# Performance work log

Measured on AMD Instinct MI355X. Metric: run time of the kernel, lower is better.

The kernel has to match this reference:

```python
import jax, jax.numpy as jnp
import numpy as np

SR = 16000
N_FFT = 400
HOP = 160
N_MELS = 128
F_MIN = 0.0
F_MAX = 8000.0
PCEN_ALPHA = 0.8
PCEN_SMOOTH = 0.04
PCEN_DELTA = 2.0
PCEN_ROOT = 2.0
PCEN_FLOOR = 1e-08
TARGET = (192, 128)


def _hz_to_mel(f):
    return 2595.0 * np.log10(1.0 + f / 700.0)


def _mel_to_hz(m):
    return 700.0 * (10.0 ** (m / 2595.0) - 1.0)


def _mel_filterbank():
    # torchaudio melscale_fbanks, mel_scale='htk', norm=None
    n_freqs = N_FFT // 2 + 1  # 201
    all_freqs = np.linspace(0.0, SR / 2, n_freqs)
    m_pts = np.linspace(_hz_to_mel(F_MIN), _hz_to_mel(F_MAX), N_MELS + 2)
    f_pts = _mel_to_hz(m_pts)
    f_diff = f_pts[1:] - f_pts[:-1]  # (n_mels+1,)
    slopes = f_pts[None, :] - all_freqs[:, None]  # (n_freqs, n_mels+2)
    down = -slopes[:, :-2] / f_diff[:-1]
    up = slopes[:, 2:] / f_diff[1:]
    fb = np.maximum(0.0, np.minimum(down, up))  # (n_freqs, n_mels)
    return jnp.asarray(fb, dtype=jnp.float32)


def _hann_window():
    # periodic hann, matches torch.hann_window(400)
    n = np.arange(N_FFT)
    return jnp.asarray(0.5 * (1.0 - np.cos(2.0 * np.pi * n / N_FFT)), dtype=jnp.float32)


def setup_inputs() -> dict:
    key = jax.random.key(0)
    audio = jax.random.normal(key, (2048, 32000), dtype=jnp.float32)
    return {"audio": audio}


def _mel_spectrogram(audio):
    # center=True reflect pad by n_fft//2
    pad = N_FFT // 2
    x = jnp.pad(audio, ((0, 0), (pad, pad)), mode='reflect')  # (N, 32400)
    T = (x.shape[1] - N_FFT) // HOP + 1  # 201
    idx = jnp.arange(T)[:, None] * HOP + jnp.arange(N_FFT)[None, :]  # (T, n_fft)
    frames = x[:, idx] * _hann_window()  # (N, T, n_fft)
    spec = jnp.fft.rfft(frames, axis=-1)  # (N, T, 201)
    power = jnp.abs(spec) ** 2
    mel = jnp.einsum('ntf,fm->ntm', power, _mel_filterbank())  # (N, T, n_mels)
    return mel


def _pcen(mel_ntm):
    # IIR smoothing over time via scan; mel_ntm: (N, T, M)
    s = PCEN_SMOOTH
    mel_t = jnp.transpose(mel_ntm, (1, 0, 2))  # (T, N, M)

    def step(m_prev, e):
        m_new = (1.0 - s) * m_prev + s * e
        return m_new, m_new

    m0 = mel_t[0]
    _, Ms = jax.lax.scan(step, m0, mel_t[1:])
    M = jnp.concatenate([m0[None], Ms], axis=0)  # (T, N, Mels)
    M = jnp.transpose(M, (1, 0, 2))  # (N, T, Mels)
    inv_r = 1.0 / PCEN_ROOT
    return (mel_ntm / (PCEN_FLOOR + M) ** PCEN_ALPHA + PCEN_DELTA) ** inv_r - PCEN_DELTA ** inv_r


def reference(audio):
    mel = _mel_spectrogram(audio)          # (N, T, 128); original is (N,128,T), PCEN over time either way
    pcen = _pcen(mel)                      # (N, T, 128) == original after transpose(1,2)
    x = pcen[:, None, :, :]                # (N, 1, T, 128)
    N = x.shape[0]
    # bilinear, align_corners=False == jax.image 'linear' (half-pixel centers)
    out = jax.image.resize(x, (N, 1, TARGET[0], TARGET[1]), method='linear')
    return out
```

## Files before the change

kernel.cpp:

```cpp
#include <hip/hip_runtime.h>
#include <math.h>

typedef __attribute__((ext_vector_type(8))) _Float16 half8;
typedef __attribute__((ext_vector_type(4))) float f32x4;
typedef __attribute__((ext_vector_type(4))) unsigned int u32x4;

namespace {
constexpr int NS = 32000, PAD = 200, NT = 201, TOUT = 192, NMEL = 128;
constexpr int PW_STRIDE = 236;
constexpr int BAS_NT = 28;
constexpr int BAS_ELEMS = 13 * 28 * 64 * 8;
constexpr int FB_ELEMS  = 7 * 8 * 64 * 8;
constexpr int OUT_ROW_U16 = TOUT * NMEL * 2;
constexpr int MEL_OFF_U16 = OUT_ROW_U16 - NT * NMEL;
}

__device__ __forceinline__ int swz(int e) { return e ^ (((e >> 7) & 3) << 3); }
__device__ __forceinline__ unsigned short f2h(float f) {
  _Float16 h = (_Float16)f; return __builtin_bit_cast(unsigned short, h);
}
__device__ __forceinline__ float h2f(unsigned short u) {
  return (float)__builtin_bit_cast(_Float16, u);
}

__global__ void setup_tables(unsigned short* __restrict__ ws) {
  int idx = blockIdx.x * 256 + threadIdx.x;
  if (idx < BAS_ELEMS) {
    int j = idx & 7, lane = (idx >> 3) & 63, rest = idx >> 9;
    int nt = rest % BAS_NT, ks = rest / BAS_NT;
    int k   = ks * 32 + ((lane >> 4) << 3) + j;
    int col = nt * 16 + (lane & 15);
    float v = 0.f;
    if (k < 400 && col < 402) {
      int bin = col >> 1;
      int mm  = (k * bin) % 400;
      float th = (float)mm * 0.015707963267948967f;
      float tr = (col & 1) ? sinf(th) : cosf(th);
      float wn = 0.5f * (1.0f - cosf((float)k * 0.015707963267948967f));
      v = wn * tr;
    }
    ws[idx] = f2h(v);
  } else if (idx < BAS_ELEMS + FB_ELEMS) {
    int i2 = idx - BAS_ELEMS;
    int j = i2 & 7, lane = (i2 >> 3) & 63, rest = i2 >> 9;
    int nt = rest % 8, ks = rest / 8;
    int k   = ks * 32 + ((lane >> 4) << 3) + j;
    int mel = nt * 16 + (lane & 15);
    float v = 0.f;
    if (k <= 200) {
      double mhi = 2595.0 * log10(1.0 + 8000.0 / 700.0);
      double ml = mhi * (double)mel / 129.0;
      double mc = mhi * (double)(mel + 1) / 129.0;
      double mr = mhi * (double)(mel + 2) / 129.0;
      double fl = 700.0 * (pow(10.0, ml / 2595.0) - 1.0);
      double fc = 700.0 * (pow(10.0, mc / 2595.0) - 1.0);
      double fr = 700.0 * (pow(10.0, mr / 2595.0) - 1.0);
      double f  = 40.0 * (double)k;
      double wv = fmin((f - fl) / (fc - fl), (fr - f) / (fr - fc));
      v = (float)fmax(0.0, wv);
    }
    ws[idx] = f2h(v);
  }
}

template <int MT>
__global__ __launch_bounds__(256) __attribute__((amdgpu_waves_per_eu(3)))
void dft_mel_kernel(const float* __restrict__ audio, const unsigned short* __restrict__ ws,
                    unsigned short* __restrict__ outu)
{
  constexpr int AU = (MT == 3) ? 7936 : 2816;
  __shared__ unsigned short au[AU];
  __shared__ unsigned short pw16[MT * 16 * PW_STRIDE];
  const int tid = threadIdx.x;
  const int bid = blockIdx.x;
  const int r  = (MT == 3) ? (bid >> 2) : bid;
  const int t0 = (MT == 3) ? ((bid & 3) * 48) : 192;
  const float* __restrict__ ab = audio + (size_t)r * NS;
  const int g0 = t0 * 160 - PAD;

  {
    constexpr int nchunk = AU / 8;
    #pragma unroll 4
    for (int ci = tid; ci < nchunk; ci += 256) {
      half8 hv;
      int gbase = g0 + ci * 8;
      if (gbase >= 0 && gbase + 7 < NS) {
        const float4* p = (const float4*)(ab + gbase);
        float4 x0 = p[0], x1 = p[1];
        hv[0] = (_Float16)x0.x; hv[1] = (_Float16)x0.y;
        hv[2] = (_Float16)x0.z; hv[3] = (_Float16)x0.w;
        hv[4] = (_Float16)x1.x; hv[5] = (_Float16)x1.y;
        hv[6] = (_Float16)x1.z; hv[7] = (_Float16)x1.w;
      } else {
        #pragma unroll
        for (int j = 0; j < 8; ++j) {
          int g = gbase + j;
          if (g < 0) g = -g;
          if (g >= NS) g = 2 * NS - 2 - g;
          hv[j] = (_Float16)ab[g];
        }
      }
      *(half8*)(au + swz(ci * 8)) = hv;
    }
  }
  __syncthreads();

  const int w = tid >> 6, lane = tid & 63, lr = lane & 15, lg = lane >> 4;

  f32x4 acc[MT][7];
  #pragma unroll
  for (int mm = 0; mm < MT; ++mm)
    #pragma unroll
    for (int n = 0; n < 7; ++n) acc[mm][n] = (f32x4){0.f, 0.f, 0.f, 0.f};
  {
    const int laneA = lr * 160 + lg * 8;
    const unsigned short* bptr = ws + ((size_t)(w * 7 * 64 + lane)) * 8;
    half8 Bcur = *(const half8*)bptr;
    for (int ks = 0; ks < 13; ++ks) {
      half8 Af[MT];
      #pragma unroll
      for (int mm = 0; mm < MT; ++mm)
        Af[mm] = *(const half8*)(au + swz(mm * 2560 + ks * 32 + laneA));
      #pragma unroll
      for (int n = 0; n < 7; ++n) {
        half8 Bnext = Bcur;
        if (n < 6)        Bnext = *(const half8*)(bptr + (n + 1) * 512);
        else if (ks < 12) Bnext = *(const half8*)(bptr + BAS_NT * 512);
        #pragma unroll
        for (int mm = 0; mm < MT; ++mm)
          acc[mm][n] = __builtin_amdgcn_mfma_f32_16x16x32_f16(Af[mm], Bcur, acc[mm][n], 0, 0, 0);
        Bcur = Bnext;
      }
      bptr += BAS_NT * 512;
    }
  }
  __syncthreads();

  #pragma unroll
  for (int mm = 0; mm < MT; ++mm) {
    #pragma unroll
    for (int n = 0; n < 7; ++n) {
      int gcol = (w * 7 + n) * 16 + lr;
      int bin  = gcol >> 1;
      float p[4];
      #pragma unroll
      for (int j = 0; j < 4; ++j) {
        float v = acc[mm][n][j];
        int iv = __builtin_bit_cast(int, v);
        float q = __builtin_bit_cast(float,
            __builtin_amdgcn_mov_dpp(iv, 0xB1, 0xF, 0xF, true));
        p[j] = fmaf(v, v, q * q);
      }
      bool odd = (lr & 1);
      int rowb = mm * 16 + lg * 4 + (odd ? 2 : 0);
      pw16[rowb * PW_STRIDE + bin]       = f2h(odd ? p[2] : p[0]);
      pw16[(rowb + 1) * PW_STRIDE + bin] = f2h(odd ? p[3] : p[1]);
    }
  }
  __syncthreads();

  {
    half8 Fb[2][7];
    const unsigned short* fbase = ws + BAS_ELEMS + (size_t)lane * 8;
    #pragma unroll
    for (int nt = 0; nt < 2; ++nt)
      #pragma unroll
      for (int ks = 0; ks < 7; ++ks)
        Fb[nt][ks] = *(const half8*)(fbase + ((size_t)(ks * 8 + 2 * w + nt)) * 512);
    #pragma unroll
    for (int mt = 0; mt < MT; ++mt) {
      half8 Pa[7];
      const unsigned short* psrc = pw16 + (mt * 16 + lr) * PW_STRIDE + lg * 8;
      #pragma unroll
      for (int ks = 0; ks < 7; ++ks) Pa[ks] = *(const half8*)(psrc + ks * 32);
      #pragma unroll
      for (int nt = 0; nt < 2; ++nt) {
        f32x4 a2 = (f32x4){0.f, 0.f, 0.f, 0.f};
        #pragma unroll
        for (int ks = 0; ks < 7; ++ks)
          a2 = __builtin_amdgcn_mfma_f32_16x16x32_f16(Pa[ks], Fb[nt][ks], a2, 0, 0, 0);
        int gm = (2 * w + nt) * 16 + lr;
        #pragma unroll
        for (int j = 0; j < 4; ++j) {
          int t = t0 + mt * 16 + lg * 4 + j;
          if (MT == 3 || t < NT)
            outu[(size_t)r * OUT_ROW_U16 + MEL_OFF_U16 + t * NMEL + gm] = f2h(a2[j]);
        }
      }
    }
  }
}

__global__ __launch_bounds__(512)
void pcen_resize_kernel(unsigned short* __restrict__ outu)
{
  __shared__ unsigned short mel[NT * NMEL];
  __shared__ float carry[4][NMEL];
  __shared__ float minb[4][NMEL];
  const int tid = threadIdx.x;
  const int r = blockIdx.x;
  const unsigned short* src = outu + (size_t)r * OUT_ROW_U16 + MEL_OFF_U16;
  for (int i = tid; i < (NT * NMEL) / 8; i += 512)
    *(u32x4*)(mel + i * 8) = *(const u32x4*)(src + (size_t)i * 8);
  __syncthreads();

  const int m = tid & 127, c = tid >> 7;
  const int t0  = (c == 0) ? 0 : (51 + 50 * (c - 1));
  const int len = (c == 0) ? 51 : 50;

  float M = 0.f;
  for (int t = t0; t < t0 + len; ++t) {
    float e = h2f(mel[t * NMEL + m]);
    M = (t == 0) ? e : fmaf(0.96f, M, 0.04f * e);
  }
  carry[c][m] = M;
  __syncthreads();
  if (c == 0) {
    float a50 = exp2f(50.0f * log2f(0.96f));
    float m1 = carry[0][m];
    float m2 = fmaf(a50, m1, carry[1][m]);
    float m3 = fmaf(a50, m2, carry[2][m]);
    minb[1][m] = m1; minb[2][m] = m2; minb[3][m] = m3;
  }
  __syncthreads();

  float Min = (c == 0) ? 0.f : minb[c][m];
  float wf = 1.f, Mloc = 0.f;
  for (int t = t0; t < t0 + len; ++t) {
    float e = h2f(mel[t * NMEL + m]);
    Mloc = (t == 0) ? e : fmaf(0.96f, Mloc, 0.04f * e);
    wf *= 0.96f;
    float Mt = fmaf(wf, Min, Mloc);
    float dn = exp2f(0.8f * log2f(1e-8f + Mt));
    float pc = sqrtf(e / dn + 2.0f) - 1.41421356237309515f;
    mel[t * NMEL + m] = f2h(pc);
  }
  __syncthreads();

  float* __restrict__ ob = (float*)outu + (size_t)r * TOUT * NMEL;
  const float INVS = 201.0f / 192.0f;
  for (int i = c; i < TOUT; i += 4) {
    float ct = ((float)i + 0.5f) * INVS - 0.5f;
    int jlo = (int)ceilf(ct - INVS);
    int jhi = (int)floorf(ct + INVS);
    if (jlo < 0) jlo = 0;
    if (jhi > NT - 1) jhi = NT - 1;
    float wsum = 0.f, val = 0.f;
    for (int j = jlo; j <= jhi; ++j) {
      float wv = 1.0f - fabsf((float)j - ct) / INVS;
      if (wv > 0.f) { wsum += wv; val = fmaf(wv, h2f(mel[j * NMEL + m]), val); }
    }
    ob[(size_t)i * NMEL + m] = val / wsum;
  }
}

extern "C" void kernel_launch(void* const* d_in, const int* in_sizes, int n_in,
                              void* d_out, int out_size, void* d_ws, size_t ws_size,
                              hipStream_t stream) {
  (void)in_sizes; (void)n_in; (void)out_size; (void)ws_size;
  unsigned short* ws = (unsigned short*)d_ws;
  setup_tables<<<(BAS_ELEMS + FB_ELEMS + 255) / 256, 256, 0, stream>>>(ws);
  dft_mel_kernel<3><<<2048 * 4, 256, 0, stream>>>((const float*)d_in[0], ws,
                                                  (unsigned short*)d_out);
  dft_mel_kernel<1><<<2048, 256, 0, stream>>>((const float*)d_in[0], ws,
                                              (unsigned short*)d_out);
  pcen_resize_kernel<<<2048, 512, 0, stream>>>((unsigned short*)d_out);
}
```

Before: 464.7 us.

## Merge DFT-mel launches into one kernel with aliased LDS; widen PCEN scan

The two templated DFT/mel launches (one for the 48-frame tiles, one for the tail frames) become a single launch of 5 blocks per row, dispatching on block index. The audio staging buffer and the power buffer now share one LDS allocation, which cuts shared memory per block. The amdgpu_waves_per_eu(3) attribute is dropped, which may change register allocation. The PCEN/resize kernel moves from 512 to 1024 threads, splitting the time scan into 8 chunks with a longer carry-propagation chain, to expose more parallelism per row.

Result: faster. 454.3 us (-2.2%).

```diff
diff --git a/kernel.cpp b/kernel.cpp
--- a/kernel.cpp
+++ b/kernel.cpp
@@ -13,6 +13,7 @@
 constexpr int FB_ELEMS  = 7 * 8 * 64 * 8;
 constexpr int OUT_ROW_U16 = TOUT * NMEL * 2;
 constexpr int MEL_OFF_U16 = OUT_ROW_U16 - NT * NMEL;
+constexpr int BUF_U16 = 48 * PW_STRIDE;
 }
 
 __device__ __forceinline__ int swz(int e) { return e ^ (((e >> 7) & 3) << 3); }
@@ -64,18 +65,11 @@
 }
 
 template <int MT>
-__global__ __launch_bounds__(256) __attribute__((amdgpu_waves_per_eu(3)))
-void dft_mel_kernel(const float* __restrict__ audio, const unsigned short* __restrict__ ws,
-                    unsigned short* __restrict__ outu)
+__device__ __forceinline__ void dft_mel_body(const float* __restrict__ ab,
+    const unsigned short* __restrict__ ws, unsigned short* __restrict__ outrow,
+    unsigned short* __restrict__ buf, int t0, int tid)
 {
   constexpr int AU = (MT == 3) ? 7936 : 2816;
-  __shared__ unsigned short au[AU];
-  __shared__ unsigned short pw16[MT * 16 * PW_STRIDE];
-  const int tid = threadIdx.x;
-  const int bid = blockIdx.x;
-  const int r  = (MT == 3) ? (bid >> 2) : bid;
-  const int t0 = (MT == 3) ? ((bid & 3) * 48) : 192;
-  const float* __restrict__ ab = audio + (size_t)r * NS;
   const int g0 = t0 * 160 - PAD;
 
   {
@@ -100,7 +94,7 @@
           hv[j] = (_Float16)ab[g];
         }
       }
-      *(half8*)(au + swz(ci * 8)) = hv;
+      *(half8*)(buf + swz(ci * 8)) = hv;
     }
   }
   __syncthreads();
@@ -120,7 +114,7 @@
       half8 Af[MT];
       #pragma unroll
       for (int mm = 0; mm < MT; ++mm)
-        Af[mm] = *(const half8*)(au + swz(mm * 2560 + ks * 32 + laneA));
+        Af[mm] = *(const half8*)(buf + swz(mm * 2560 + ks * 32 + laneA));
       #pragma unroll
       for (int n = 0; n < 7; ++n) {
         half8 Bnext = Bcur;
@@ -136,6 +130,7 @@
   }
   __syncthreads();
 
+  unsigned short* pw16 = buf;
   #pragma unroll
   for (int mm = 0; mm < MT; ++mm) {
     #pragma unroll
@@ -184,29 +179,42 @@
         for (int j = 0; j < 4; ++j) {
           int t = t0 + mt * 16 + lg * 4 + j;
           if (MT == 3 || t < NT)
-            outu[(size_t)r * OUT_ROW_U16 + MEL_OFF_U16 + t * NMEL + gm] = f2h(a2[j]);
+            outrow[t * NMEL + gm] = f2h(a2[j]);
         }
       }
     }
   }
 }
 
-__global__ __launch_bounds__(512)
+__global__ __launch_bounds__(256)
+void dft_mel_kernel(const float* __restrict__ audio, const unsigned short* __restrict__ ws,
+                    unsigned short* __restrict__ outu)
+{
+  __shared__ unsigned short buf[BUF_U16];
+  const int bid = blockIdx.x;
+  const int r = bid / 5, s = bid - r * 5;
+  const float* __restrict__ ab = audio + (size_t)r * NS;
+  unsigned short* outrow = outu + (size_t)r * OUT_ROW_U16 + MEL_OFF_U16;
+  if (s < 4) dft_mel_body<3>(ab, ws, outrow, buf, s * 48, threadIdx.x);
+  else       dft_mel_body<1>(ab, ws, outrow, buf, 192, threadIdx.x);
+}
+
+__global__ __launch_bounds__(1024)
 void pcen_resize_kernel(unsigned short* __restrict__ outu)
 {
   __shared__ unsigned short mel[NT * NMEL];
-  __shared__ float carry[4][NMEL];
-  __shared__ float minb[4][NMEL];
+  __shared__ float carry[8][NMEL];
+  __shared__ float minb[8][NMEL];
   const int tid = threadIdx.x;
   const int r = blockIdx.x;
   const unsigned short* src = outu + (size_t)r * OUT_ROW_U16 + MEL_OFF_U16;
-  for (int i = tid; i < (NT * NMEL) / 8; i += 512)
+  for (int i = tid; i < (NT * NMEL) / 8; i += 1024)
     *(u32x4*)(mel + i * 8) = *(const u32x4*)(src + (size_t)i * 8);
   __syncthreads();
 
   const int m = tid & 127, c = tid >> 7;
-  const int t0  = (c == 0) ? 0 : (51 + 50 * (c - 1));
-  const int len = (c == 0) ? 51 : 50;
+  const int t0  = (c == 0) ? 0 : (26 + 25 * (c - 1));
+  const int len = (c == 0) ? 26 : 25;
 
   float M = 0.f;
   for (int t = t0; t < t0 + len; ++t) {
@@ -216,11 +224,14 @@
   carry[c][m] = M;
   __syncthreads();
   if (c == 0) {
-    float a50 = exp2f(50.0f * log2f(0.96f));
-    float m1 = carry[0][m];
-    float m2 = fmaf(a50, m1, carry[1][m]);
-    float m3 = fmaf(a50, m2, carry[2][m]);
-    minb[1][m] = m1; minb[2][m] = m2; minb[3][m] = m3;
+    float a25 = exp2f(25.0f * log2f(0.96f));
+    float acc = carry[0][m];
+    minb[1][m] = acc;
+    #pragma unroll
+    for (int cc = 2; cc < 8; ++cc) {
+      acc = fmaf(a25, acc, carry[cc - 1][m]);
+      minb[cc][m] = acc;
+    }
   }
   __syncthreads();
 
@@ -239,7 +250,7 @@
 
   float* __restrict__ ob = (float*)outu + (size_t)r * TOUT * NMEL;
   const float INVS = 201.0f / 192.0f;
-  for (int i = c; i < TOUT; i += 4) {
+  for (int i = c; i < TOUT; i += 8) {
     float ct = ((float)i + 0.5f) * INVS - 0.5f;
     int jlo = (int)ceilf(ct - INVS);
     int jhi = (int)floorf(ct + INVS);
@@ -260,9 +271,7 @@
   (void)in_sizes; (void)n_in; (void)out_size; (void)ws_size;
   unsigned short* ws = (unsigned short*)d_ws;
   setup_tables<<<(BAS_ELEMS + FB_ELEMS + 255) / 256, 256, 0, stream>>>(ws);
-  dft_mel_kernel<3><<<2048 * 4, 256, 0, stream>>>((const float*)d_in[0], ws,
-                                                  (unsigned short*)d_out);
-  dft_mel_kernel<1><<<2048, 256, 0, stream>>>((const float*)d_in[0], ws,
-                                              (unsigned short*)d_out);
-  pcen_resize_kernel<<<2048, 512, 0, stream>>>((unsigned short*)d_out);
-}
+  dft_mel_kernel<<<2048 * 5, 256, 0, stream>>>((const float*)d_in[0], ws,
+                                               (unsigned short*)d_out);
+  pcen_resize_kernel<<<2048, 1024, 0, stream>>>((unsigned short*)d_out);
+}
```
